# Performance work log

Measured on AMD Instinct MI355X. Metric: run time of the kernel, lower is better.

Reference implementation:

```python
import jax, jax.numpy as jnp
import numpy as np
from jax import lax

VOCAB = 50000; WD = 50; PD = 5; PV = 201  # pos vocab = 2*100+1
HID = 230; REL = 53; L = 120
BAGS = 512; B = 8; N = BAGS * B; QL = 8; EL = 2


def setup_inputs():
    key = jax.random.key(0)
    k = list(jax.random.split(key, 16))
    ar = jnp.arange(BAGS)
    return {
        "X": jax.random.randint(k[0], (N, L), 0, VOCAB),
        "X_Pos1": jax.random.randint(k[1], (N, L), 0, PV),
        "X_Pos2": jax.random.randint(k[2], (N, L), 0, PV),
        "E1": jax.random.randint(k[3], (BAGS * EL,), 0, VOCAB),
        "E2": jax.random.randint(k[4], (BAGS * EL,), 0, VOCAB),
        "X_Mask": jnp.zeros((N, L), jnp.int32),
        "X_Len": jnp.full((N,), L, jnp.int32),
        "X_Scope": jnp.stack([ar * B, ar * B + B], 1),
        "Scope_ent1": jnp.stack([ar * EL, ar * EL + EL], 1),
        "Scope_ent2": jnp.stack([ar * EL, ar * EL + EL], 1),
        "Q": jax.random.randint(k[5], (BAGS, QL), 0, VOCAB),
        "X_Rel": jax.random.randint(k[6], (BAGS,), 0, REL),
        "W_word": 0.1 * jax.random.normal(k[7], (VOCAB, WD), jnp.float32),
        "W_pos1": 0.1 * jax.random.normal(k[8], (PV, PD), jnp.float32),
        "W_pos2": 0.1 * jax.random.normal(k[9], (PV, PD), jnp.float32),
        "w_s": 0.1 * jax.random.normal(k[10], (WD,), jnp.float32),
        "b_s": jnp.zeros((), jnp.float32),
        "w_q": 0.1 * jax.random.normal(k[11], (WD,), jnp.float32),
        "b_q": jnp.zeros((), jnp.float32),
        "w_sq": 0.1 * jax.random.normal(k[12], (WD,), jnp.float32),
        "b_sq": jnp.zeros((), jnp.float32),
        "conv_W": 0.05 * jax.random.normal(k[13], (3, 3 * WD + 2 * PD, HID), jnp.float32),
        "conv_b": jnp.zeros((HID,), jnp.float32),
        "rel_W": 0.1 * jax.random.normal(k[14], (REL, HID), jnp.float32),
        "rel_b": jnp.zeros((REL,), jnp.float32),
    }


def _forward(X, X_Pos1, X_Pos2, E1, E2, Q, X_Rel,
             W_word, W_pos1, W_pos2, w_s, b_s, w_q, b_q, w_sq, b_sq,
             conv_W, conv_b, rel_W, rel_b):
    s = W_word[X]            # [N, L, WD]
    p1 = W_pos1[X_Pos1]      # [N, L, PD]
    p2 = W_pos2[X_Pos2]
    # query embedding: mean entity-mention embeddings into template slots -4 / -2
    e1 = W_word[E1].reshape(BAGS, EL, WD).mean(1)
    e2 = W_word[E2].reshape(BAGS, EL, WD).mean(1)
    q = W_word[Q].at[:, -4].set(e1).at[:, -2].set(e2)  # [BAGS, QL, WD]
    q = jnp.repeat(q, B, axis=0)                        # [N, QL, WD] per-bag repeat
    # BiDAF-style similarity h[n, l, j]
    sq = jnp.einsum('nld,d,njd->nlj', s, w_sq, q) + b_sq
    h = (s @ w_s + b_s)[:, :, None] + (q @ w_q + b_q)[:, None, :] + sq
    a = jax.nn.softmax(h, axis=2)
    s2q = jnp.einsum('nlj,njd->nld', a, q)              # [N, L, WD]
    b_att = jax.nn.softmax(h.max(axis=2), axis=1)       # [N, L]
    q2s = jnp.einsum('nl,nld->nd', b_att, s)            # [N, WD]
    x = jnp.concatenate([s, s * s2q, s * q2s[:, None, :], p1, p2], -1)  # [N, L, 160]
    # CNN encoder: conv1d k=3 SAME, max-over-time, relu
    y = lax.conv_general_dilated(x, conv_W, (1,), 'SAME',
                                 dimension_numbers=('NWC', 'WIO', 'NWC')) + conv_b
    enc = jax.nn.relu(y.max(axis=1))                    # [N, HID]
    # bag self-attention (dropout disabled, eval mode)
    bag = enc.reshape(BAGS, B, HID)
    att = jax.nn.softmax(jnp.einsum('bnd,bmd->bnm', bag, bag) / np.sqrt(HID).astype(np.float32), axis=-1)
    bag = jnp.einsum('bnm,bmd->bnd', att, bag)
    # sentence attention with gold relation query (training branch)
    relv = rel_W[X_Rel]                                 # [BAGS, HID]
    score = jax.nn.softmax(jnp.einsum('bnd,bd->bn', bag, relv), axis=1)
    rep = jnp.einsum('bn,bnd->bd', score, bag)          # [BAGS, HID]
    return rep @ rel_W.T + rel_b                        # [BAGS, REL]


def reference(X, X_Pos1, X_Pos2, E1, E2, X_Mask, X_Len, X_Scope, Scope_ent1, Scope_ent2, Q, X_Rel,
              W_word, W_pos1, W_pos2, w_s, b_s, w_q, b_q, w_sq, b_sq, conv_W, conv_b, rel_W, rel_b):
    # X_Mask / X_Len are PCNN/RNN-encoder inputs, unused by the CNN path.
    # X_Scope / Scope_ent* encode uniform bags (B=8) and mention spans (EL=2),
    # realized here as static reshapes.
    return _forward(X, X_Pos1, X_Pos2, E1, E2, Q, X_Rel,
                    W_word, W_pos1, W_pos2, w_s, b_s, w_q, b_q, w_sq, b_sq,
                    conv_W, conv_b, rel_W, rel_b)
```

## Files before the change

### kernel.cpp

```cpp
#include <hip/hip_runtime.h>
#include <hip/hip_bf16.h>

#define WD 50
#define PD 5
#define HID 230
#define RELN 53
#define LLEN 120
#define BAGS 512
#define BB 8
#define NSENT 4096
#define QL 8
#define CIN 160
#define KTOT 480
#define XROW 168
#define XROWS 130

typedef __attribute__((ext_vector_type(4))) float f32x4;
typedef __attribute__((ext_vector_type(8))) short short8;

__device__ __forceinline__ float bf2f(short u) {
    union { float f; unsigned int i; } v;
    v.i = ((unsigned int)(unsigned short)u) << 16;
    return v.f;
}
__device__ __forceinline__ short f2bf(float f) {
    union { float f; unsigned int i; } v; v.f = f;
    unsigned int r = v.i + 0x7FFFu + ((v.i >> 16) & 1u);
    return (short)(r >> 16);
}

__global__ void build_q_kernel(const int* __restrict__ Q, const int* __restrict__ E1,
                               const int* __restrict__ E2, const float* __restrict__ W_word,
                               float* __restrict__ q_ws) {
    int b = blockIdx.x;
    int d = threadIdx.x;
    if (d >= WD) return;
    float e1 = 0.5f * (W_word[E1[2 * b] * WD + d] + W_word[E1[2 * b + 1] * WD + d]);
    float e2 = 0.5f * (W_word[E2[2 * b] * WD + d] + W_word[E2[2 * b + 1] * WD + d]);
    for (int j = 0; j < QL; ++j) {
        float v;
        if (j == QL - 4)      v = e1;
        else if (j == QL - 2) v = e2;
        else                  v = W_word[Q[b * QL + j] * WD + d];
        q_ws[(b * QL + j) * WD + d] = v;
    }
}

__global__ void pack_w_kernel(const float* __restrict__ conv_W, short* __restrict__ wt2) {
    int i = blockIdx.x * 256 + threadIdx.x;
    if (i >= 15 * 256 * 32) return;
    int ks = i >> 13, rem = i & 8191;
    int row = rem >> 5, kk = rem & 31;
    int k = ks * 32 + kk;
    float v = (row < HID) ? conv_W[k * HID + row] : 0.f;
    wt2[i] = f2bf(v);
}

__launch_bounds__(512, 4)
__global__ void sent_kernel(const int* __restrict__ X, const int* __restrict__ XP1,
                            const int* __restrict__ XP2,
                            const float* __restrict__ W_word,
                            const float* __restrict__ W_pos1, const float* __restrict__ W_pos2,
                            const float* __restrict__ w_s, const float* __restrict__ b_s,
                            const float* __restrict__ w_q, const float* __restrict__ b_q,
                            const float* __restrict__ w_sq, const float* __restrict__ b_sq,
                            const float* __restrict__ conv_b,
                            const float* __restrict__ q_ws, const short* __restrict__ wt2,
                            float* __restrict__ enc) {
    extern __shared__ char smem[];
    short* xl  = (short*)smem;
    short* qtb = xl + XROWS * XROW;
    short* abf = qtb + 64 * 32;
    short* qwb = abf + 136 * 8;
    short* hm  = qwb + 16 * 64;
    float* svv = (float*)(hm + LLEN * 8);
    float* bat = svv + LLEN;
    float* qsv = bat + LLEN;
    float* smax = qsv + 8;
    float* red  = smax + 512;

    const int tid = threadIdx.x;
    const int n = blockIdx.x;
    const int bag = n >> 3;
    const int lane = tid & 63;
    const int wid = tid >> 6;
    const int r16 = lane & 15;
    const int g = lane >> 4;

    {
        int* xli = (int*)xl;
        for (int i = tid; i < 840; i += 512) {
            int rs = i / 84, col = i % 84;
            int row = (rs == 0) ? 0 : 120 + rs;
            xli[row * 84 + col] = 0;
        }
        for (int i = tid; i < 840; i += 512) {
            int row = 1 + i / 7, ci = 25 + i % 7;
            xli[row * 84 + ci] = 0;
        }
        int* abfi = (int*)abf;
        if (tid < 64) abfi[120 * 4 + tid] = 0;
        int* qtbi = (int*)qtb;
        for (int i = tid; i < 1024; i += 512) qtbi[i] = 0;
    }
    for (int i = tid; i < LLEN * 25; i += 512) {
        int l = i / 25, dp = i % 25;
        const float2 v = *(const float2*)(W_word + X[n * LLEN + l] * WD + dp * 2);
        unsigned int pk = ((unsigned int)(unsigned short)f2bf(v.y) << 16)
                        | (unsigned short)f2bf(v.x);
        *(unsigned int*)(xl + (l + 1) * XROW + dp * 2) = pk;
    }
    for (int i = tid; i < LLEN * 2 * PD; i += 512) {
        int l = i / 10, c = i % 10;
        float v = (c < PD) ? W_pos1[XP1[n * LLEN + l] * PD + c]
                           : W_pos2[XP2[n * LLEN + l] * PD + (c - PD)];
        xl[(l + 1) * XROW + 150 + c] = f2bf(v);
    }
    __syncthreads();
    if (tid < WD) {
        short8 v;
        for (int j = 0; j < QL; ++j) v[j] = f2bf(q_ws[(bag * QL + j) * WD + tid]);
        *(short8*)(qtb + tid * 32) = v;
    }
    if (tid >= 64 && tid < 64 + 72) {
        int t = tid - 64, j = t >> 3, g8 = t & 7;
        short8 v;
        for (int e = 0; e < 8; ++e) {
            int c = g8 * 8 + e;
            float x = 0.f;
            if (c < WD) x = (j < 8) ? q_ws[(bag * QL + j) * WD + c] * w_sq[c] : w_s[c];
            v[e] = f2bf(x);
        }
        *(short8*)(qwb + j * 64 + g8 * 8) = v;
    }
    if (tid >= 504) {
        int j = tid - 504;
        float acc = b_q[0];
        for (int d = 0; d < WD; ++d) acc += q_ws[(bag * QL + j) * WD + d] * w_q[d];
        qsv[j] = acc;
    }
    __syncthreads();

    {
        const float bsq = b_sq[0], bs = b_s[0];
        f32x4 hacc = (f32x4){0.f, 0.f, 0.f, 0.f};
        for (int ks2 = 0; ks2 < 2; ++ks2) {
            short8 af = *(const short8*)(xl + (1 + 16 * wid + r16) * XROW + ks2 * 32 + g * 8);
            short8 bf = *(const short8*)(qwb + r16 * 64 + ks2 * 32 + g * 8);
            hacc = __builtin_amdgcn_mfma_f32_16x16x32_bf16(af, bf, hacc, 0, 0, 0);
        }
        if (r16 < QL) {
            float qs = qsv[r16] + bsq;
            for (int r = 0; r < 4; ++r) {
                int l = 16 * wid + 4 * g + r;
                if (l < LLEN) hm[l * 8 + r16] = f2bf(hacc[r] + qs);
            }
        } else if (r16 == QL) {
            for (int r = 0; r < 4; ++r) {
                int l = 16 * wid + 4 * g + r;
                if (l < LLEN) svv[l] = hacc[r] + bs;
            }
        }
    }
    __syncthreads();

    if (tid < LLEN) {
        const int l = tid;
        short8 hrow = *(const short8*)(hm + l * 8);
        float a[8], m = -1e30f;
        for (int j = 0; j < 8; ++j) { a[j] = bf2f(hrow[j]); m = fmaxf(m, a[j]); }
        float sum = 0.f;
        for (int j = 0; j < 8; ++j) { a[j] = expf(a[j] - m); sum += a[j]; }
        float inv = 1.f / sum;
        short8 arow;
        for (int j = 0; j < 8; ++j) arow[j] = f2bf(a[j] * inv);
        *(short8*)(abf + l * 8) = arow;
        bat[l] = expf(m + svv[l]);
    }
    __syncthreads();

    if (tid < 400) {
        int c = tid / WD, d = tid % WD;
        float acc = 0.f;
        for (int l = c * 15; l < c * 15 + 15; ++l)
            acc += bat[l] * bf2f(xl[(l + 1) * XROW + d]);
        smax[c * 52 + d] = acc;
    } else if (tid >= 448) {
        int ln = tid - 448;
        float v = (ln < LLEN ? bat[ln] : 0.f) + (ln + 64 < LLEN ? bat[ln + 64] : 0.f);
        for (int o = 32; o >= 1; o >>= 1) v += __shfl_xor(v, o, 64);
        if (ln == 0) red[0] = v;
    }
    __syncthreads();

    {
        float rinv = 1.0f / red[0];
        short8 af = *(const short8*)(abf + (16 * wid + r16) * 8 + g * 8);
        for (int nt = 0; nt < 4; ++nt) {
            short8 bf = *(const short8*)(qtb + (16 * nt + r16) * 32 + g * 8);
            f32x4 acc2 = __builtin_amdgcn_mfma_f32_16x16x32_bf16(
                af, bf, (f32x4){0.f, 0.f, 0.f, 0.f}, 0, 0, 0);
            int d = 16 * nt + r16;
            if (d < WD) {
                float q2sd = 0.f;
                for (int c = 0; c < 8; ++c) q2sd += smax[c * 52 + d];
                q2sd *= rinv;
                for (int r = 0; r < 4; ++r) {
                    int l = 16 * wid + 4 * g + r;
                    if (l < LLEN) {
                        short* row = xl + (l + 1) * XROW;
                        float s = bf2f(row[d]);
                        row[50 + d]  = f2bf(s * acc2[r]);
                        row[100 + d] = f2bf(s * q2sd);
                    }
                }
            }
        }
    }
    __syncthreads();

    const int wm = wid >> 2;
    const int wn = wid & 3;
    f32x4 acc[4][4];
    for (int a = 0; a < 4; ++a)
        for (int b2 = 0; b2 < 4; ++b2) acc[a][b2] = (f32x4){0.f, 0.f, 0.f, 0.f};

    const short* wb = wt2 + (64 * wn + r16) * 32 + g * 8;
    const int arow0 = 64 * wm + r16;

    short8 b0[4], b1[4];
#pragma unroll
    for (int nf = 0; nf < 4; ++nf) b0[nf] = *(const short8*)(wb + nf * 512);

#pragma unroll 1
    for (int ks = 0; ks < 14; ks += 2) {
#pragma unroll
        for (int nf = 0; nf < 4; ++nf)
            b1[nf] = *(const short8*)(wb + (ks + 1) * 8192 + nf * 512);
        {
            const int tap = ks / 5;
            const int c0 = (ks % 5) * 32 + g * 8;
#pragma unroll
            for (int mf = 0; mf < 4; ++mf) {
                short8 afr = *(const short8*)(xl + (arow0 + 16 * mf + tap) * XROW + c0);
#pragma unroll
                for (int nf = 0; nf < 4; ++nf)
                    acc[mf][nf] = __builtin_amdgcn_mfma_f32_16x16x32_bf16(
                        afr, b0[nf], acc[mf][nf], 0, 0, 0);
            }
        }
#pragma unroll
        for (int nf = 0; nf < 4; ++nf)
            b0[nf] = *(const short8*)(wb + (ks + 2) * 8192 + nf * 512);
        {
            const int ks1 = ks + 1;
            const int tap = ks1 / 5;
            const int c0 = (ks1 % 5) * 32 + g * 8;
#pragma unroll
            for (int mf = 0; mf < 4; ++mf) {
                short8 afr = *(const short8*)(xl + (arow0 + 16 * mf + tap) * XROW + c0);
#pragma unroll
                for (int nf = 0; nf < 4; ++nf)
                    acc[mf][nf] = __builtin_amdgcn_mfma_f32_16x16x32_bf16(
                        afr, b1[nf], acc[mf][nf], 0, 0, 0);
            }
        }
    }
    {
        const int tap = 2;
        const int c0 = 4 * 32 + g * 8;
#pragma unroll
        for (int mf = 0; mf < 4; ++mf) {
            short8 afr = *(const short8*)(xl + (arow0 + 16 * mf + tap) * XROW + c0);
#pragma unroll
            for (int nf = 0; nf < 4; ++nf)
                acc[mf][nf] = __builtin_amdgcn_mfma_f32_16x16x32_bf16(
                    afr, b0[nf], acc[mf][nf], 0, 0, 0);
        }
    }

    for (int nf = 0; nf < 4; ++nf) {
        float m = -1e30f;
        for (int mf = 0; mf < 4; ++mf) {
            int lbase = 64 * wm + 16 * mf + 4 * g;
            for (int r = 0; r < 4; ++r)
                if (lbase + r < LLEN) m = fmaxf(m, acc[mf][nf][r]);
        }
        m = fmaxf(m, __shfl_xor(m, 16, 64));
        m = fmaxf(m, __shfl_xor(m, 32, 64));
        if (lane < 16) smax[wm * 256 + 64 * wn + 16 * nf + lane] = m;
    }
    __syncthreads();
    for (int h = tid; h < HID; h += 512) {
        float v = fmaxf(smax[h], smax[256 + h]) + conv_b[h];
        enc[n * HID + h] = fmaxf(v, 0.f);
    }
}

__global__ void bag_kernel(const float* __restrict__ enc, const int* __restrict__ X_Rel,
                           const float* __restrict__ rel_W, const float* __restrict__ rel_b,
                           float* __restrict__ out) {
    __shared__ float bagv[BB][232];
    __shared__ float bag2[BB][232];
    __shared__ float att[BB][BB];
    __shared__ float relv[232];
    __shared__ float repv[232];
    __shared__ float sc[BB], sc2[BB];
    const int b = blockIdx.x, t = threadIdx.x;

    for (int i = t; i < BB * HID; i += 256) {
        int r = i / HID, d = i % HID;
        bagv[r][d] = enc[(b * BB + r) * HID + d];
    }
    __syncthreads();
    if (t < 64) {
        int i = t >> 3, j = t & 7;
        float acc = 0.f;
        for (int d = 0; d < HID; ++d) acc += bagv[i][d] * bagv[j][d];
        att[i][j] = acc * (1.0f / sqrtf(230.0f));
    }
    __syncthreads();
    if (t < 8) {
        float m = att[t][0];
        for (int j = 1; j < 8; ++j) m = fmaxf(m, att[t][j]);
        float e[8], s = 0.f;
        for (int j = 0; j < 8; ++j) { e[j] = expf(att[t][j] - m); s += e[j]; }
        float inv = 1.f / s;
        for (int j = 0; j < 8; ++j) att[t][j] = e[j] * inv;
    }
    __syncthreads();
    for (int i = t; i < BB * HID; i += 256) {
        int r = i / HID, d = i % HID;
        float acc = 0.f;
        for (int j = 0; j < 8; ++j) acc += att[r][j] * bagv[j][d];
        bag2[r][d] = acc;
    }
    if (t < HID) relv[t] = rel_W[X_Rel[b] * HID + t];
    __syncthreads();
    if (t < 8) {
        float acc = 0.f;
        for (int d = 0; d < HID; ++d) acc += bag2[t][d] * relv[d];
        sc[t] = acc;
    }
    __syncthreads();
    if (t < 8) {
        float m = sc[0];
        for (int j = 1; j < 8; ++j) m = fmaxf(m, sc[j]);
        sc2[t] = expf(sc[t] - m);
    }
    __syncthreads();
    if (t < HID) {
        float sum = 0.f;
        for (int j = 0; j < 8; ++j) sum += sc2[j];
        float acc = 0.f;
        for (int j = 0; j < 8; ++j) acc += sc2[j] * bag2[j][t];
        repv[t] = acc / sum;
    }
    __syncthreads();
    if (t < RELN) {
        float acc = rel_b[t];
        for (int d = 0; d < HID; ++d) acc += repv[d] * rel_W[t * HID + d];
        out[b * RELN + t] = acc;
    }
}

extern "C" void kernel_launch(void* const* d_in, const int* in_sizes, int n_in,
                              void* d_out, int out_size, void* d_ws, size_t ws_size,
                              hipStream_t stream) {
    const int* X       = (const int*)d_in[0];
    const int* XP1     = (const int*)d_in[1];
    const int* XP2     = (const int*)d_in[2];
    const int* E1      = (const int*)d_in[3];
    const int* E2      = (const int*)d_in[4];
    const int* Q       = (const int*)d_in[10];
    const int* X_Rel   = (const int*)d_in[11];
    const float* W_word = (const float*)d_in[12];
    const float* W_pos1 = (const float*)d_in[13];
    const float* W_pos2 = (const float*)d_in[14];
    const float* w_s   = (const float*)d_in[15];
    const float* b_s   = (const float*)d_in[16];
    const float* w_q   = (const float*)d_in[17];
    const float* b_q   = (const float*)d_in[18];
    const float* w_sq  = (const float*)d_in[19];
    const float* b_sq  = (const float*)d_in[20];
    const float* conv_W = (const float*)d_in[21];
    const float* conv_b = (const float*)d_in[22];
    const float* rel_W = (const float*)d_in[23];
    const float* rel_b = (const float*)d_in[24];
    float* out = (float*)d_out;

    char* ws = (char*)d_ws;
    float* q_ws = (float*)ws;
    float* enc  = q_ws + BAGS * QL * WD;
    short* wt2  = (short*)(enc + NSENT * HID);

    build_q_kernel<<<BAGS, 64, 0, stream>>>(Q, E1, E2, W_word, q_ws);
    pack_w_kernel<<<480, 256, 0, stream>>>(conv_W, wt2);

    const size_t lds_bytes =
        (size_t)XROWS * XROW * 2
        + 64 * 32 * 2
        + 136 * 8 * 2
        + 16 * 64 * 2
        + LLEN * 8 * 2
        + 4 * (LLEN + LLEN + 8 + 512 + 1);
    sent_kernel<<<NSENT, 512, lds_bytes, stream>>>(
        X, XP1, XP2, W_word, W_pos1, W_pos2,
        w_s, b_s, w_q, b_q, w_sq, b_sq, conv_b, q_ws, wt2, enc);

    bag_kernel<<<BAGS, 256, 0, stream>>>(enc, X_Rel, rel_W, rel_b, out);
}
```

Baseline: 230.1 us.

## Split conv GEMM into two N passes and shrink LDS to raise occupancy

The sentence kernel's conv MFMA loop now runs as two sequential passes, each over half the output-channel fragments. This halves the accumulator and weight-register footprint and lets launch bounds request 6 waves per EU instead of 4. LDS use also shrinks: the padded input tile drops 8 rows, and the max-reduction buffer is aliased onto the dead query-weight region, so more blocks can fit per CU. In exchange, A-fragments are read from LDS twice, and padded reads past row 121 now land in neighbouring LDS data that only feeds masked outputs.

After: 206.4 us. 1.11x faster.

```diff
diff --git a/kernel.cpp b/kernel.cpp
--- a/kernel.cpp
+++ b/kernel.cpp
@@ -13,7 +13,7 @@
 #define CIN 160
 #define KTOT 480
 #define XROW 168
-#define XROWS 130
+#define XROWS 122
 
 typedef __attribute__((ext_vector_type(4))) float f32x4;
 typedef __attribute__((ext_vector_type(8))) short short8;
@@ -56,7 +56,7 @@
     wt2[i] = f2bf(v);
 }
 
-__launch_bounds__(512, 4)
+__launch_bounds__(512, 6)
 __global__ void sent_kernel(const int* __restrict__ X, const int* __restrict__ XP1,
                             const int* __restrict__ XP2,
                             const float* __restrict__ W_word,
@@ -76,7 +76,7 @@
     float* svv = (float*)(hm + LLEN * 8);
     float* bat = svv + LLEN;
     float* qsv = bat + LLEN;
-    float* smax = qsv + 8;
+    float* smax = (float*)qwb;
     float* red  = smax + 512;
 
     const int tid = threadIdx.x;
@@ -89,9 +89,9 @@
 
     {
         int* xli = (int*)xl;
-        for (int i = tid; i < 840; i += 512) {
+        for (int i = tid; i < 168; i += 512) {
             int rs = i / 84, col = i % 84;
-            int row = (rs == 0) ? 0 : 120 + rs;
+            int row = (rs == 0) ? 0 : 121;
             xli[row * 84 + col] = 0;
         }
         for (int i = tid; i < 840; i += 512) {
@@ -221,74 +221,73 @@
 
     const int wm = wid >> 2;
     const int wn = wid & 3;
-    f32x4 acc[4][4];
-    for (int a = 0; a < 4; ++a)
-        for (int b2 = 0; b2 < 4; ++b2) acc[a][b2] = (f32x4){0.f, 0.f, 0.f, 0.f};
-
-    const short* wb = wt2 + (64 * wn + r16) * 32 + g * 8;
-    const int arow0 = 64 * wm + r16;
-
-    short8 b0[4], b1[4];
-#pragma unroll
-    for (int nf = 0; nf < 4; ++nf) b0[nf] = *(const short8*)(wb + nf * 512);
+    const int m0 = 64 * wm + r16;
+    const short* wbase = wt2 + (64 * wn + r16) * 32 + g * 8;
 
 #pragma unroll 1
-    for (int ks = 0; ks < 14; ks += 2) {
-#pragma unroll
-        for (int nf = 0; nf < 4; ++nf)
-            b1[nf] = *(const short8*)(wb + (ks + 1) * 8192 + nf * 512);
+    for (int p = 0; p < 2; ++p) {
+        f32x4 acc[4][2];
+        for (int a = 0; a < 4; ++a) {
+            acc[a][0] = (f32x4){0.f, 0.f, 0.f, 0.f};
+            acc[a][1] = (f32x4){0.f, 0.f, 0.f, 0.f};
+        }
+        const short* wb = wbase + p * 1024;
+        short8 b0[2], b1[2];
+        b0[0] = *(const short8*)(wb);
+        b0[1] = *(const short8*)(wb + 512);
+
+#pragma unroll 1
+        for (int ks = 0; ks < 14; ks += 2) {
+            b1[0] = *(const short8*)(wb + (ks + 1) * 8192);
+            b1[1] = *(const short8*)(wb + (ks + 1) * 8192 + 512);
+            {
+                const int tap = ks / 5;
+                const int c0 = (ks % 5) * 32 + g * 8;
+#pragma unroll
+                for (int mf = 0; mf < 4; ++mf) {
+                    short8 afr = *(const short8*)(xl + (m0 + 16 * mf + tap) * XROW + c0);
+                    acc[mf][0] = __builtin_amdgcn_mfma_f32_16x16x32_bf16(afr, b0[0], acc[mf][0], 0, 0, 0);
+                    acc[mf][1] = __builtin_amdgcn_mfma_f32_16x16x32_bf16(afr, b0[1], acc[mf][1], 0, 0, 0);
+                }
+            }
+            b0[0] = *(const short8*)(wb + (ks + 2) * 8192);
+            b0[1] = *(const short8*)(wb + (ks + 2) * 8192 + 512);
+            {
+                const int ks1 = ks + 1;
+                const int tap = ks1 / 5;
+                const int c0 = (ks1 % 5) * 32 + g * 8;
+#pragma unroll
+                for (int mf = 0; mf < 4; ++mf) {
+                    short8 afr = *(const short8*)(xl + (m0 + 16 * mf + tap) * XROW + c0);
+                    acc[mf][0] = __builtin_amdgcn_mfma_f32_16x16x32_bf16(afr, b1[0], acc[mf][0], 0, 0, 0);
+                    acc[mf][1] = __builtin_amdgcn_mfma_f32_16x16x32_bf16(afr, b1[1], acc[mf][1], 0, 0, 0);
+                }
+            }
+        }
         {
-            const int tap = ks / 5;
-            const int c0 = (ks % 5) * 32 + g * 8;
+            const int tap = 2;
+            const int c0 = 128 + g * 8;
 #pragma unroll
             for (int mf = 0; mf < 4; ++mf) {
-                short8 afr = *(const short8*)(xl + (arow0 + 16 * mf + tap) * XROW + c0);
-#pragma unroll
-                for (int nf = 0; nf < 4; ++nf)
-                    acc[mf][nf] = __builtin_amdgcn_mfma_f32_16x16x32_bf16(
-                        afr, b0[nf], acc[mf][nf], 0, 0, 0);
-            }
-        }
-#pragma unroll
-        for (int nf = 0; nf < 4; ++nf)
-            b0[nf] = *(const short8*)(wb + (ks + 2) * 8192 + nf * 512);
-        {
-            const int ks1 = ks + 1;
-            const int tap = ks1 / 5;
-            const int c0 = (ks1 % 5) * 32 + g * 8;
+                short8 afr = *(const short8*)(xl + (m0 + 16 * mf + tap) * XROW + c0);
+                acc[mf][0] = __builtin_amdgcn_mfma_f32_16x16x32_bf16(afr, b0[0], acc[mf][0], 0, 0, 0);
+                acc[mf][1] = __builtin_amdgcn_mfma_f32_16x16x32_bf16(afr, b0[1], acc[mf][1], 0, 0, 0);
+            }
+        }
+#pragma unroll
+        for (int nf = 0; nf < 2; ++nf) {
+            float m = -1e30f;
 #pragma unroll
             for (int mf = 0; mf < 4; ++mf) {
-                short8 afr = *(const short8*)(xl + (arow0 + 16 * mf + tap) * XROW + c0);
-#pragma unroll
-                for (int nf = 0; nf < 4; ++nf)
-                    acc[mf][nf] = __builtin_amdgcn_mfma_f32_16x16x32_bf16(
-                        afr, b1[nf], acc[mf][nf], 0, 0, 0);
-            }
-        }
-    }
-    {
-        const int tap = 2;
-        const int c0 = 4 * 32 + g * 8;
-#pragma unroll
-        for (int mf = 0; mf < 4; ++mf) {
-            short8 afr = *(const short8*)(xl + (arow0 + 16 * mf + tap) * XROW + c0);
-#pragma unroll
-            for (int nf = 0; nf < 4; ++nf)
-                acc[mf][nf] = __builtin_amdgcn_mfma_f32_16x16x32_bf16(
-                    afr, b0[nf], acc[mf][nf], 0, 0, 0);
-        }
-    }
-
-    for (int nf = 0; nf < 4; ++nf) {
-        float m = -1e30f;
-        for (int mf = 0; mf < 4; ++mf) {
-            int lbase = 64 * wm + 16 * mf + 4 * g;
-            for (int r = 0; r < 4; ++r)
-                if (lbase + r < LLEN) m = fmaxf(m, acc[mf][nf][r]);
-        }
-        m = fmaxf(m, __shfl_xor(m, 16, 64));
-        m = fmaxf(m, __shfl_xor(m, 32, 64));
-        if (lane < 16) smax[wm * 256 + 64 * wn + 16 * nf + lane] = m;
+                int lbase = 64 * wm + 16 * mf + 4 * g;
+#pragma unroll
+                for (int r = 0; r < 4; ++r)
+                    if (lbase + r < LLEN) m = fmaxf(m, acc[mf][nf][r]);
+            }
+            m = fmaxf(m, __shfl_xor(m, 16, 64));
+            m = fmaxf(m, __shfl_xor(m, 32, 64));
+            if (lane < 16) smax[wm * 256 + 64 * wn + 32 * p + 16 * nf + r16] = m;
+        }
     }
     __syncthreads();
     for (int h = tid; h < HID; h += 512) {
@@ -403,7 +402,7 @@
         + 136 * 8 * 2
         + 16 * 64 * 2
         + LLEN * 8 * 2
-        + 4 * (LLEN + LLEN + 8 + 512 + 1);
+        + 4 * (LLEN + LLEN + 8);
     sent_kernel<<<NSENT, 512, lds_bytes, stream>>>(
         X, XP1, XP2, W_word, W_pos1, W_pos2,
         w_s, b_s, w_q, b_q, w_sq, b_sq, conv_b, q_ws, wt2, enc);
```
